# Kernel tuning notes

Measured on AMD Instinct MI355X. Metric: run time of the kernel, lower is better.

The kernel has to match this reference:

```python
import jax, jax.numpy as jnp
import numpy as np

B, S, D, U, L, DEG = 32, 256, 256, 256, 16, 16
N = B * S
E = N * DEG


def _xavier(k, shape, fan_in, fan_out):
    return jax.random.normal(k, shape, jnp.float32) * np.float32(np.sqrt(2.0 / (fan_in + fan_out)))


def setup_inputs() -> dict:
    key = jax.random.key(0)
    ks = jax.random.split(key, 16)
    src = jax.random.normal(ks[0], (S, B, D), jnp.float32)
    V_in = _xavier(ks[1], (L, D, U), D, U)
    b_in = jnp.zeros((L, U), jnp.float32)
    V_in_gate = _xavier(ks[2], (D, 1), D, 1)
    b_in_gate = jnp.ones((L, 1), jnp.float32)
    V_out = _xavier(ks[3], (L, D, U), D, U)
    b_out = jnp.zeros((L, U), jnp.float32)
    V_out_gate = _xavier(ks[4], (D, 1), D, 1)
    b_out_gate = jnp.ones((L, 1), jnp.float32)
    W_self_loop = _xavier(ks[5], (D, U), D, U)
    W_self_loop_gate = _xavier(ks[6], (D, 1), D, 1)
    arc_tensor_in = jnp.stack([jax.random.randint(ks[7], (E,), 0, B),
                               jax.random.randint(ks[8], (E,), 0, S)]).astype(jnp.int64)
    arc_tensor_out = jnp.stack([jax.random.randint(ks[9], (E,), 0, B),
                                jax.random.randint(ks[10], (E,), 0, S)]).astype(jnp.int64)
    label_tensor_in = jax.random.randint(ks[11], (1, E), 0, L).astype(jnp.int64)
    label_tensor_out = jax.random.randint(ks[12], (1, E), 0, L).astype(jnp.int64)
    mask_in = jnp.ones((N, DEG), jnp.float32)
    mask_out = jnp.ones((N, DEG), jnp.float32)
    mask_loop = jnp.ones((N, 1), jnp.float32)
    sent_mask = jnp.ones((S, B), jnp.float32)
    return {"src": src, "V_in": V_in, "b_in": b_in, "V_in_gate": V_in_gate,
            "b_in_gate": b_in_gate, "V_out": V_out, "b_out": b_out,
            "V_out_gate": V_out_gate, "b_out_gate": b_out_gate,
            "W_self_loop": W_self_loop, "W_self_loop_gate": W_self_loop_gate,
            "arc_tensor_in": arc_tensor_in, "arc_tensor_out": arc_tensor_out,
            "label_tensor_in": label_tensor_in, "label_tensor_out": label_tensor_out,
            "mask_in": mask_in, "mask_out": mask_out, "mask_loop": mask_loop,
            "sent_mask": sent_mask}


def _gcn_forward(src, V_in, b_in, V_in_gate, b_in_gate, V_out, b_out, V_out_gate,
                 b_out_gate, W_self_loop, W_self_loop_gate, mask_in, mask_out,
                 mask_loop, sent_mask, arc_tensor_in, arc_tensor_out,
                 label_tensor_in, label_tensor_out):
    S_, B_, D_ = src.shape
    U_ = V_in.shape[-1]
    enc = jnp.transpose(src, (1, 0, 2))            # [B,S,D]
    x = enc.reshape(B_ * S_, D_)                   # [N,D]

    def arc_branch(V, b, Vg, bg, arc, lab):
        # per-label transform of all nodes, as in the original: [L,N,U]
        all_lab = jnp.einsum('nd,ldu->lnu', x, V)
        idx = arc[0] * S_ + arc[1]                 # [E] flat node indices
        l = lab[0]                                  # [E] edge labels
        feats = all_lab[l, idx] + b[l]              # [E,U]
        deg = idx.shape[0] // (B_ * S_)
        feats = feats.reshape(B_, S_, deg, U_)
        g = (x @ Vg)[idx, 0] + bg[l, 0]             # [E]
        gate = g.reshape(B_, S_, deg)
        return feats, gate

    in_, in_gate = arc_branch(V_in, b_in, V_in_gate, b_in_gate, arc_tensor_in, label_tensor_in)
    out_, out_gate = arc_branch(V_out, b_out, V_out_gate, b_out_gate, arc_tensor_out, label_tensor_out)
    same = (x @ W_self_loop).reshape(B_, S_, 1, U_)
    same_gate = (x @ W_self_loop_gate).reshape(B_, S_, 1)

    pot = jnp.concatenate([in_, out_, same], axis=2)            # [B,S,maxdeg,U]
    pot_gate = jnp.concatenate([in_gate, out_gate, same_gate], axis=2)
    mask_soft = jnp.concatenate([mask_in, mask_out, mask_loop], axis=1)  # [N,maxdeg]
    md = pot.shape[2]
    pot = pot.reshape(B_ * S_, md, U_)
    probs = jax.nn.sigmoid(pot_gate.reshape(B_ * S_, md)) * mask_soft
    res = jax.nn.relu(jnp.sum(pot * probs[:, :, None], axis=1)).reshape(B_, S_, U_)
    res = res * sent_mask.T[:, :, None]
    return jnp.transpose(res, (1, 0, 2))            # [S,B,U]


def reference(src, V_in, b_in, V_in_gate, b_in_gate, V_out, b_out, V_out_gate,
              b_out_gate, W_self_loop, W_self_loop_gate, arc_tensor_in,
              arc_tensor_out, label_tensor_in, label_tensor_out, mask_in,
              mask_out, mask_loop, sent_mask):
    return _gcn_forward(src, V_in, b_in, V_in_gate, b_in_gate, V_out, b_out,
                        V_out_gate, b_out_gate, W_self_loop, W_self_loop_gate,
                        mask_in, mask_out, mask_loop, sent_mask,
                        arc_tensor_in, arc_tensor_out, label_tensor_in,
                        label_tensor_out)
```

## Files before the change

### kernel.cpp

```cpp
#include <hip/hip_runtime.h>
#include <hip/hip_bf16.h>

#define BB 32
#define SS 256
#define DD 256
#define UU 256
#define LL 16
#define DEG 16
#define NN (BB * SS)
#define EE (NN * DEG)
#define NSLICE 33
#define KMAIN (NSLICE * DD)
#define KTOT  (KMAIN + 128)
#define KSPLIT 4
#define KS (KTOT / KSPLIT)

using short8 = __attribute__((ext_vector_type(8))) short;
using f32x4  = __attribute__((ext_vector_type(4))) float;

#define GLDS(g, l)                                                        \
  __builtin_amdgcn_global_load_lds(                                       \
      (const __attribute__((address_space(1))) void*)(g),                 \
      (__attribute__((address_space(3))) void*)(l), 16, 0, 0)

__device__ __forceinline__ float bf2f(unsigned short v) {
  union { unsigned u; float f; } t;
  t.u = ((unsigned)v) << 16;
  return t.f;
}
__device__ __forceinline__ float sigm(float x) {
  return 1.f / (1.f + __expf(-x));
}

__global__ __launch_bounds__(256) void k_prep(
    const float* __restrict__ src, const float* __restrict__ gin,
    const float* __restrict__ gout, const float* __restrict__ gloop,
    __hip_bfloat16* __restrict__ x_bf, float* __restrict__ xg_in,
    float* __restrict__ xg_out, float* __restrict__ xg_loop) {
  int n = blockIdx.x;
  int b = n / SS, s = n % SS;
  int d = threadIdx.x;
  float v = src[(size_t)(s * BB + b) * DD + d];
  x_bf[(size_t)n * DD + d] = __float2bfloat16(v);
  float p0 = v * gin[d], p1 = v * gout[d], p2 = v * gloop[d];
#pragma unroll
  for (int o = 32; o > 0; o >>= 1) {
    p0 += __shfl_down(p0, o);
    p1 += __shfl_down(p1, o);
    p2 += __shfl_down(p2, o);
  }
  __shared__ float r0[4], r1[4], r2[4];
  int w = threadIdx.x >> 6, lane = threadIdx.x & 63;
  if (lane == 0) { r0[w] = p0; r1[w] = p1; r2[w] = p2; }
  __syncthreads();
  if (threadIdx.x == 0) {
    xg_in[n]   = r0[0] + r0[1] + r0[2] + r0[3];
    xg_out[n]  = r1[0] + r1[1] + r1[2] + r1[3];
    xg_loop[n] = r2[0] + r2[1] + r2[2] + r2[3];
  }
}

__global__ void k_transpose(const float* __restrict__ Vin,
                            const float* __restrict__ Vout,
                            const float* __restrict__ Wself,
                            __hip_bfloat16* __restrict__ Vt) {
  __shared__ float t[32][33];
  int z = blockIdx.z;
  const float* srcM = (z == 0) ? Wself
                    : (z <= LL ? Vin  + (size_t)(z - 1)      * DD * UU
                               : Vout + (size_t)(z - 1 - LL) * DD * UU);
  int u0 = blockIdx.x * 32, d0 = blockIdx.y * 32;
  int tx = threadIdx.x, ty = threadIdx.y;
#pragma unroll
  for (int i = 0; i < 4; i++) {
    int dr = ty + i * 8;
    t[dr][tx] = srcM[(size_t)(d0 + dr) * UU + u0 + tx];
  }
  __syncthreads();
#pragma unroll
  for (int i = 0; i < 4; i++) {
    int ur = ty + i * 8;
    Vt[(size_t)(u0 + ur) * KTOT + z * DD + d0 + tx] = __float2bfloat16(t[tx][ur]);
  }
}

__global__ __launch_bounds__(128) void k_biasfill(
    const float* __restrict__ b_in, const float* __restrict__ b_out,
    __hip_bfloat16* __restrict__ Vt) {
  int u = blockIdx.x, j = threadIdx.x;
  float v = 0.f;
  if (j >= 1 && j <= LL)       v = b_in[(j - 1) * UU + u];
  else if (j > LL && j < NSLICE) v = b_out[(j - 1 - LL) * UU + u];
  Vt[(size_t)u * KTOT + KMAIN + j] = __float2bfloat16(v);
}

__global__ __launch_bounds__(256) void k_agg(
    const __hip_bfloat16* __restrict__ x,
    const float* __restrict__ xg_in, const float* __restrict__ xg_out,
    const float* __restrict__ xg_loop,
    const float* __restrict__ b_ing, const float* __restrict__ b_outg,
    const int* __restrict__ arc_in, const int* __restrict__ arc_out,
    const int* __restrict__ lab_in, const int* __restrict__ lab_out,
    const float* __restrict__ mask_in, const float* __restrict__ mask_out,
    const float* __restrict__ mask_loop,
    __hip_bfloat16* __restrict__ Y) {
  __shared__ float Ya[NSLICE][DD];
  __shared__ int s_src[32];
  __shared__ int s_sl[32];
  __shared__ float s_w[32];
  __shared__ float s_wsum[NSLICE];
  int n = blockIdx.x, tid = threadIdx.x;
  if (tid < 32) {
    int br = tid >> 4, k = tid & 15;
    int e = n * DEG + k;
    const int* a = br ? arc_out : arc_in;
    int l = (br ? lab_out : lab_in)[e];
    int srcn = a[e] * SS + a[EE + e];
    float g = (br ? xg_out : xg_in)[srcn] + (br ? b_outg : b_ing)[l];
    s_src[tid] = srcn;
    s_sl[tid] = 1 + br * LL + l;
    s_w[tid] = sigm(g) * (br ? mask_out : mask_in)[e];
  }
  __syncthreads();
  float wl = sigm(xg_loop[n]) * mask_loop[n];
  Ya[0][tid] = wl * bf2f(((const unsigned short*)x)[(size_t)n * DD + tid]);
#pragma unroll
  for (int i = 1; i < NSLICE; i++) Ya[i][tid] = 0.f;
#pragma unroll 4
  for (int k = 0; k < 32; k++) {
    float wv = s_w[k];
    float xv = bf2f(((const unsigned short*)x)[(size_t)s_src[k] * DD + tid]);
    Ya[s_sl[k]][tid] += wv * xv;
  }
  if (tid < NSLICE) {
    float ws = 0.f;
#pragma unroll
    for (int k = 0; k < 32; k++) ws += (s_sl[k] == tid) ? s_w[k] : 0.f;
    s_wsum[tid] = ws;
  }
  __syncthreads();
  size_t base = (size_t)n * KTOT;
#pragma unroll
  for (int i = 0; i < NSLICE; i++)
    Y[base + i * DD + tid] = __float2bfloat16(Ya[i][tid]);
  if (tid < 128)
    Y[base + KMAIN + tid] = __float2bfloat16(tid < NSLICE ? s_wsum[tid] : 0.f);
}

__global__ __launch_bounds__(256) void k_gemm(
    const __hip_bfloat16* __restrict__ A, const __hip_bfloat16* __restrict__ Bt,
    float* __restrict__ partial) {
  __shared__ __align__(16) __hip_bfloat16 As[128 * 32];
  __shared__ __align__(16) __hip_bfloat16 Bs[128 * 32];
  float* P = partial + (size_t)blockIdx.z * NN * UU;
  int kbeg = blockIdx.z * KS;

  int row0 = blockIdx.x * 128, col0 = blockIdx.y * 128;
  int tid = threadIdx.x;
  int w = tid >> 6, lane = tid & 63;
  int wr = (w >> 1) * 64, wc = (w & 1) * 64;
  int lrow = lane & 15, quad = lane >> 4;
  int sr = lane >> 2;
  int sc = (lane & 3) * 8;

  f32x4 acc[4][4] = {};
  for (int k0 = kbeg; k0 < kbeg + KS; k0 += 32) {
#pragma unroll
    for (int t = 0; t < 2; t++) {
      int rb = (w * 2 + t) * 16;
      GLDS(&A[(size_t)(row0 + rb + sr) * KTOT + k0 + sc], &As[rb * 32]);
      GLDS(&Bt[(size_t)(col0 + rb + sr) * KTOT + k0 + sc], &Bs[rb * 32]);
    }
    __syncthreads();
    short8 af[4], bfr[4];
#pragma unroll
    for (int i = 0; i < 4; i++)
      af[i] = *(const short8*)&As[(wr + i * 16 + lrow) * 32 + quad * 8];
#pragma unroll
    for (int j = 0; j < 4; j++)
      bfr[j] = *(const short8*)&Bs[(wc + j * 16 + lrow) * 32 + quad * 8];
#pragma unroll
    for (int i = 0; i < 4; i++)
#pragma unroll
      for (int j = 0; j < 4; j++)
        acc[i][j] = __builtin_amdgcn_mfma_f32_16x16x32_bf16(af[i], bfr[j], acc[i][j], 0, 0, 0);
    __syncthreads();
  }
#pragma unroll
  for (int i = 0; i < 4; i++)
#pragma unroll
    for (int j = 0; j < 4; j++) {
      int col = col0 + wc + j * 16 + lrow;
      int rowb = row0 + wr + i * 16 + quad * 4;
#pragma unroll
      for (int r = 0; r < 4; r++)
        P[(size_t)(rowb + r) * UU + col] = acc[i][j][r];
    }
}

__global__ __launch_bounds__(64) void k_finish(const float* __restrict__ partial,
                                               const float* __restrict__ sent,
                                               float* __restrict__ out) {
  int n = blockIdx.x, u4 = threadIdx.x * 4;
  size_t idx = (size_t)n * UU + u4;
  float4 a = *(const float4*)&partial[idx];
#pragma unroll
  for (int z = 1; z < KSPLIT; z++) {
    float4 b = *(const float4*)&partial[(size_t)z * NN * UU + idx];
    a.x += b.x; a.y += b.y; a.z += b.z; a.w += b.w;
  }
  int s = n % SS, b = n / SS;
  float sm = sent[s * BB + b];
  float4 o;
  o.x = fmaxf(a.x, 0.f) * sm; o.y = fmaxf(a.y, 0.f) * sm;
  o.z = fmaxf(a.z, 0.f) * sm; o.w = fmaxf(a.w, 0.f) * sm;
  *(float4*)&out[((size_t)s * BB + b) * UU + u4] = o;
}

extern "C" void kernel_launch(void* const* d_in, const int* in_sizes, int n_in,
                              void* d_out, int out_size, void* d_ws, size_t ws_size,
                              hipStream_t stream) {
  const float* src      = (const float*)d_in[0];
  const float* V_in     = (const float*)d_in[1];
  const float* b_in     = (const float*)d_in[2];
  const float* V_ing    = (const float*)d_in[3];
  const float* b_ing    = (const float*)d_in[4];
  const float* V_out    = (const float*)d_in[5];
  const float* b_out    = (const float*)d_in[6];
  const float* V_outg   = (const float*)d_in[7];
  const float* b_outg   = (const float*)d_in[8];
  const float* W_self   = (const float*)d_in[9];
  const float* W_selfg  = (const float*)d_in[10];
  const int* arc_in     = (const int*)d_in[11];
  const int* arc_out    = (const int*)d_in[12];
  const int* lab_in     = (const int*)d_in[13];
  const int* lab_out    = (const int*)d_in[14];
  const float* mask_in  = (const float*)d_in[15];
  const float* mask_out = (const float*)d_in[16];
  const float* mask_loop= (const float*)d_in[17];
  const float* sent     = (const float*)d_in[18];
  float* out = (float*)d_out;

  char* ws = (char*)d_ws;
  size_t off = 0;
  auto alloc = [&](size_t bytes) -> void* {
    void* p = ws + off;
    off += (bytes + 255) & ~(size_t)255;
    return p;
  };
  __hip_bfloat16* x_bf = (__hip_bfloat16*)alloc((size_t)NN * DD * 2);
  __hip_bfloat16* Vt   = (__hip_bfloat16*)alloc((size_t)UU * KTOT * 2);
  float* xg_in   = (float*)alloc(NN * 4);
  float* xg_out  = (float*)alloc(NN * 4);
  float* xg_loop = (float*)alloc(NN * 4);
  __hip_bfloat16* Y = (__hip_bfloat16*)alloc((size_t)NN * KTOT * 2);
  float* partial = (float*)alloc((size_t)KSPLIT * NN * UU * 4);

  k_prep<<<NN, 256, 0, stream>>>(src, V_ing, V_outg, W_selfg, x_bf, xg_in, xg_out, xg_loop);
  k_transpose<<<dim3(UU / 32, DD / 32, NSLICE), dim3(32, 8), 0, stream>>>(
      V_in, V_out, W_self, Vt);
  k_biasfill<<<UU, 128, 0, stream>>>(b_in, b_out, Vt);
  k_agg<<<NN, 256, 0, stream>>>(x_bf, xg_in, xg_out, xg_loop, b_ing, b_outg,
                                arc_in, arc_out, lab_in, lab_out,
                                mask_in, mask_out, mask_loop, Y);
  k_gemm<<<dim3(NN / 128, UU / 128, KSPLIT), 256, 0, stream>>>(Y, Vt, partial);
  k_finish<<<NN, 64, 0, stream>>>(partial, sent, out);
}
```

Baseline: 228.1 us.

## Sort edges by slice in aggregation, drop LDS accumulator, store bf16 split-K partials

The aggregation kernel now uses one 64-thread wavefront per node. It ranks the 32 edges by label slice and accumulates each slice in registers with 4-wide vector loads, which removes the 33x256 float LDS accumulator and lets more blocks fit per CU. Split-K rises from 4 to 8 and the K padding grows to 256. The GEMM now writes partials in bf16, halving partial traffic per split, and the finish kernel sums them in fp32. Rounding each partial to bf16 adds error, and the extra split adds GEMM launch work on a reduced K per block.

```diff
diff --git a/kernel.cpp b/kernel.cpp
--- a/kernel.cpp
+++ b/kernel.cpp
@@ -11,8 +11,9 @@
 #define EE (NN * DEG)
 #define NSLICE 33
 #define KMAIN (NSLICE * DD)
-#define KTOT  (KMAIN + 128)
-#define KSPLIT 4
+#define KEXT 256
+#define KTOT (KMAIN + KEXT)
+#define KSPLIT 8
 #define KS (KTOT / KSPLIT)
 
 using short8 = __attribute__((ext_vector_type(8))) short;
@@ -27,6 +28,10 @@
   union { unsigned u; float f; } t;
   t.u = ((unsigned)v) << 16;
   return t.f;
+}
+__device__ __forceinline__ unsigned short f2bf(float f) {
+  __hip_bfloat16 h = __float2bfloat16(f);
+  return *(unsigned short*)&h;
 }
 __device__ __forceinline__ float sigm(float x) {
   return 1.f / (1.f + __expf(-x));
@@ -84,17 +89,17 @@
   }
 }
 
-__global__ __launch_bounds__(128) void k_biasfill(
+__global__ __launch_bounds__(256) void k_biasfill(
     const float* __restrict__ b_in, const float* __restrict__ b_out,
     __hip_bfloat16* __restrict__ Vt) {
   int u = blockIdx.x, j = threadIdx.x;
   float v = 0.f;
-  if (j >= 1 && j <= LL)       v = b_in[(j - 1) * UU + u];
-  else if (j > LL && j < NSLICE) v = b_out[(j - 1 - LL) * UU + u];
+  if (j >= 1 && j <= LL)           v = b_in[(j - 1) * UU + u];
+  else if (j > LL && j < NSLICE)   v = b_out[(j - 1 - LL) * UU + u];
   Vt[(size_t)u * KTOT + KMAIN + j] = __float2bfloat16(v);
 }
 
-__global__ __launch_bounds__(256) void k_agg(
+__global__ __launch_bounds__(64) void k_agg(
     const __hip_bfloat16* __restrict__ x,
     const float* __restrict__ xg_in, const float* __restrict__ xg_out,
     const float* __restrict__ xg_loop,
@@ -104,9 +109,9 @@
     const float* __restrict__ mask_in, const float* __restrict__ mask_out,
     const float* __restrict__ mask_loop,
     __hip_bfloat16* __restrict__ Y) {
-  __shared__ float Ya[NSLICE][DD];
-  __shared__ int s_src[32];
-  __shared__ int s_sl[32];
+  __shared__ int u_sl[32], u_src[32];
+  __shared__ float u_w[32];
+  __shared__ int s_sl[32], s_src[32];
   __shared__ float s_w[32];
   __shared__ float s_wsum[NSLICE];
   int n = blockIdx.x, tid = threadIdx.x;
@@ -117,42 +122,73 @@
     int l = (br ? lab_out : lab_in)[e];
     int srcn = a[e] * SS + a[EE + e];
     float g = (br ? xg_out : xg_in)[srcn] + (br ? b_outg : b_ing)[l];
-    s_src[tid] = srcn;
-    s_sl[tid] = 1 + br * LL + l;
-    s_w[tid] = sigm(g) * (br ? mask_out : mask_in)[e];
-  }
-  __syncthreads();
-  float wl = sigm(xg_loop[n]) * mask_loop[n];
-  Ya[0][tid] = wl * bf2f(((const unsigned short*)x)[(size_t)n * DD + tid]);
-#pragma unroll
-  for (int i = 1; i < NSLICE; i++) Ya[i][tid] = 0.f;
-#pragma unroll 4
-  for (int k = 0; k < 32; k++) {
-    float wv = s_w[k];
-    float xv = bf2f(((const unsigned short*)x)[(size_t)s_src[k] * DD + tid]);
-    Ya[s_sl[k]][tid] += wv * xv;
-  }
-  if (tid < NSLICE) {
-    float ws = 0.f;
-#pragma unroll
-    for (int k = 0; k < 32; k++) ws += (s_sl[k] == tid) ? s_w[k] : 0.f;
-    s_wsum[tid] = ws;
-  }
-  __syncthreads();
+    u_sl[tid] = 1 + br * LL + l;
+    u_src[tid] = srcn;
+    u_w[tid] = sigm(g) * (br ? mask_out : mask_in)[e];
+  }
+  __syncthreads();
+  if (tid < 32) {
+    int my = u_sl[tid];
+    int rank = 0;
+#pragma unroll
+    for (int j = 0; j < 32; j++) {
+      int oj = u_sl[j];
+      rank += (oj < my || (oj == my && j < tid)) ? 1 : 0;
+    }
+    s_sl[rank] = my;
+    s_src[rank] = u_src[tid];
+    s_w[rank] = u_w[tid];
+  }
+  __syncthreads();
+
+  const unsigned short* xp = (const unsigned short*)x;
   size_t base = (size_t)n * KTOT;
-#pragma unroll
-  for (int i = 0; i < NSLICE; i++)
-    Y[base + i * DD + tid] = __float2bfloat16(Ya[i][tid]);
-  if (tid < 128)
-    Y[base + KMAIN + tid] = __float2bfloat16(tid < NSLICE ? s_wsum[tid] : 0.f);
+  int d4 = tid * 4;
+  {
+    float wl = sigm(xg_loop[n]) * mask_loop[n];
+    ushort4 v = *(const ushort4*)&xp[(size_t)n * DD + d4];
+    ushort4 o;
+    o.x = f2bf(wl * bf2f(v.x)); o.y = f2bf(wl * bf2f(v.y));
+    o.z = f2bf(wl * bf2f(v.z)); o.w = f2bf(wl * bf2f(v.w));
+    *(ushort4*)&((unsigned short*)Y)[base + d4] = o;
+  }
+  int ptr = 0;
+  for (int s = 1; s < NSLICE; s++) {
+    float a0 = 0.f, a1 = 0.f, a2 = 0.f, a3 = 0.f, ws = 0.f;
+    while (ptr < 32 && s_sl[ptr] == s) {
+      int srcn = s_src[ptr];
+      float w = s_w[ptr];
+      ushort4 v = *(const ushort4*)&xp[(size_t)srcn * DD + d4];
+      a0 += w * bf2f(v.x); a1 += w * bf2f(v.y);
+      a2 += w * bf2f(v.z); a3 += w * bf2f(v.w);
+      ws += w;
+      ptr++;
+    }
+    ushort4 o;
+    o.x = f2bf(a0); o.y = f2bf(a1); o.z = f2bf(a2); o.w = f2bf(a3);
+    *(ushort4*)&((unsigned short*)Y)[base + s * DD + d4] = o;
+    if (tid == 0) s_wsum[s] = ws;
+  }
+  __syncthreads();
+  {
+    ushort4 o;
+    unsigned short* op = (unsigned short*)&o;
+#pragma unroll
+    for (int c = 0; c < 4; c++) {
+      int j = d4 + c;
+      float v = (j >= 1 && j < NSLICE) ? s_wsum[j] : 0.f;
+      op[c] = f2bf(v);
+    }
+    *(ushort4*)&((unsigned short*)Y)[base + KMAIN + d4] = o;
+  }
 }
 
 __global__ __launch_bounds__(256) void k_gemm(
     const __hip_bfloat16* __restrict__ A, const __hip_bfloat16* __restrict__ Bt,
-    float* __restrict__ partial) {
+    __hip_bfloat16* __restrict__ partial) {
   __shared__ __align__(16) __hip_bfloat16 As[128 * 32];
   __shared__ __align__(16) __hip_bfloat16 Bs[128 * 32];
-  float* P = partial + (size_t)blockIdx.z * NN * UU;
+  __hip_bfloat16* P = partial + (size_t)blockIdx.z * NN * UU;
   int kbeg = blockIdx.z * KS;
 
   int row0 = blockIdx.x * 128, col0 = blockIdx.y * 128;
@@ -194,26 +230,27 @@
       int rowb = row0 + wr + i * 16 + quad * 4;
 #pragma unroll
       for (int r = 0; r < 4; r++)
-        P[(size_t)(rowb + r) * UU + col] = acc[i][j][r];
-    }
-}
-
-__global__ __launch_bounds__(64) void k_finish(const float* __restrict__ partial,
-                                               const float* __restrict__ sent,
-                                               float* __restrict__ out) {
+        P[(size_t)(rowb + r) * UU + col] = __float2bfloat16(acc[i][j][r]);
+    }
+}
+
+__global__ __launch_bounds__(64) void k_finish(
+    const __hip_bfloat16* __restrict__ partial, const float* __restrict__ sent,
+    float* __restrict__ out) {
   int n = blockIdx.x, u4 = threadIdx.x * 4;
   size_t idx = (size_t)n * UU + u4;
-  float4 a = *(const float4*)&partial[idx];
-#pragma unroll
-  for (int z = 1; z < KSPLIT; z++) {
-    float4 b = *(const float4*)&partial[(size_t)z * NN * UU + idx];
-    a.x += b.x; a.y += b.y; a.z += b.z; a.w += b.w;
+  const unsigned short* pp = (const unsigned short*)partial;
+  float a0 = 0.f, a1 = 0.f, a2 = 0.f, a3 = 0.f;
+#pragma unroll
+  for (int z = 0; z < KSPLIT; z++) {
+    ushort4 v = *(const ushort4*)&pp[(size_t)z * NN * UU + idx];
+    a0 += bf2f(v.x); a1 += bf2f(v.y); a2 += bf2f(v.z); a3 += bf2f(v.w);
   }
   int s = n % SS, b = n / SS;
   float sm = sent[s * BB + b];
   float4 o;
-  o.x = fmaxf(a.x, 0.f) * sm; o.y = fmaxf(a.y, 0.f) * sm;
-  o.z = fmaxf(a.z, 0.f) * sm; o.w = fmaxf(a.w, 0.f) * sm;
+  o.x = fmaxf(a0, 0.f) * sm; o.y = fmaxf(a1, 0.f) * sm;
+  o.z = fmaxf(a2, 0.f) * sm; o.w = fmaxf(a3, 0.f) * sm;
   *(float4*)&out[((size_t)s * BB + b) * UU + u4] = o;
 }
 
@@ -254,15 +291,16 @@
   float* xg_out  = (float*)alloc(NN * 4);
   float* xg_loop = (float*)alloc(NN * 4);
   __hip_bfloat16* Y = (__hip_bfloat16*)alloc((size_t)NN * KTOT * 2);
-  float* partial = (float*)alloc((size_t)KSPLIT * NN * UU * 4);
+  __hip_bfloat16* partial =
+      (__hip_bfloat16*)alloc((size_t)KSPLIT * NN * UU * 2);
 
   k_prep<<<NN, 256, 0, stream>>>(src, V_ing, V_outg, W_selfg, x_bf, xg_in, xg_out, xg_loop);
   k_transpose<<<dim3(UU / 32, DD / 32, NSLICE), dim3(32, 8), 0, stream>>>(
       V_in, V_out, W_self, Vt);
-  k_biasfill<<<UU, 128, 0, stream>>>(b_in, b_out, Vt);
-  k_agg<<<NN, 256, 0, stream>>>(x_bf, xg_in, xg_out, xg_loop, b_ing, b_outg,
-                                arc_in, arc_out, lab_in, lab_out,
-                                mask_in, mask_out, mask_loop, Y);
+  k_biasfill<<<UU, 256, 0, stream>>>(b_in, b_out, Vt);
+  k_agg<<<NN, 64, 0, stream>>>(x_bf, xg_in, xg_out, xg_loop, b_ing, b_outg,
+                               arc_in, arc_out, lab_in, lab_out,
+                               mask_in, mask_out, mask_loop, Y);
   k_gemm<<<dim3(NN / 128, UU / 128, KSPLIT), 256, 0, stream>>>(Y, Vt, partial);
   k_finish<<<NN, 64, 0, stream>>>(partial, sent, out);
 }
```

Result: faster. 211.6 us (-7.2%).
